# Optimization experiments

Hardware: AMD Instinct MI355X
Metric: run time of the kernel (lower is better)

## Reference

```python
import jax, jax.numpy as jnp
import numpy as np

EMBED = 1024
HEADS = 16
HDIM = EMBED // HEADS
MASK_OUT = -10000.0


def setup_inputs() -> dict:
    key = jax.random.key(0)
    ks = jax.random.split(key, 12)
    B, S = 4, 1023
    scale = 0.02
    return {
        "word_hidden_states": jax.random.normal(ks[0], (B, S, EMBED), jnp.float32),
        "image_hidden_states": jax.random.normal(ks[1], (B, EMBED), jnp.float32),
        "attention_mask": jnp.zeros((B, 1, 1, S), jnp.float32),
        "c_attn_w": jax.random.normal(ks[2], (EMBED, 3 * EMBED), jnp.float32) * scale,
        "c_attn_b": jnp.zeros((3 * EMBED,), jnp.float32),
        "c_proj_w": jax.random.normal(ks[3], (EMBED, EMBED), jnp.float32) * scale,
        "c_proj_b": jnp.zeros((EMBED,), jnp.float32),
        "uk_w": jax.random.normal(ks[4], (EMBED, EMBED), jnp.float32) * scale,
        "uk_b": jnp.zeros((EMBED,), jnp.float32),
        "uv_w": jax.random.normal(ks[5], (EMBED, EMBED), jnp.float32) * scale,
        "uv_b": jnp.zeros((EMBED,), jnp.float32),
    }


def _split_heads(t):
    # [B, T, E] -> [B, H, T, D]
    B, T, _ = t.shape
    return t.reshape(B, T, HEADS, HDIM).transpose(0, 2, 1, 3)


def reference(word_hidden_states, image_hidden_states, attention_mask,
              c_attn_w, c_attn_b, c_proj_w, c_proj_b,
              uk_w, uk_b, uv_w, uv_b):
    B, S, _ = word_hidden_states.shape
    # c_attn: Conv1D -> x @ W + b, then split into q, k, v
    qkv = word_hidden_states @ c_attn_w + c_attn_b          # [B, S, 3E]
    q_word, k_word, v_word = jnp.split(qkv, 3, axis=-1)
    # image key/value via nn.Linear (x @ W^T + b)
    img = image_hidden_states[:, None, :]                    # [B, 1, E]
    k_img = img @ uk_w.T + uk_b
    v_img = img @ uv_w.T + uv_b
    k = jnp.concatenate([k_img, k_word], axis=1)             # [B, S+1, E]
    v = jnp.concatenate([v_img, v_word], axis=1)

    q = _split_heads(q_word)                                 # [B, H, S, D]
    k = _split_heads(k)                                      # [B, H, S+1, D]
    v = _split_heads(v)

    scores = jnp.einsum("bhqd,bhkd->bhqk", q, k) / jnp.sqrt(jnp.float32(HDIM))
    # causal mask: tril rows [1 : S+1], cols [: S+1] of max_positions grid
    # -> query i may attend key j iff j <= i + 1 (image token always visible)
    qi = jnp.arange(S)[:, None]
    kj = jnp.arange(S + 1)[None, :]
    causal = kj <= qi + 1                                     # [S, S+1]
    scores = jnp.where(causal[None, None], scores, jnp.float32(MASK_OUT))
    # prepend zero column to additive attention mask for the image token
    zero_col = jnp.zeros(attention_mask.shape[:-1] + (1,), attention_mask.dtype)
    mask = jnp.concatenate([zero_col, attention_mask], axis=-1)  # [B,1,1,S+1]
    scores = scores + mask
    attn = jax.nn.softmax(scores, axis=-1)                    # dropout: eval mode (identity)
    out = jnp.einsum("bhqk,bhkd->bhqd", attn, v)              # [B, H, S, D]
    out = out.transpose(0, 2, 1, 3).reshape(B, S, EMBED)      # merge heads
    out = out @ c_proj_w + c_proj_b                           # c_proj Conv1D
    return out
```

## Files before the change

### kernel.cpp

```cpp
#include <hip/hip_runtime.h>

#define EMBED 1024
#define HEADS 16
#define HDIM 64
#define SQ 1023
#define SK 1024
#define MTOK 4092
#define MPAD 4096

typedef __attribute__((ext_vector_type(8))) short short8;
typedef __attribute__((ext_vector_type(4))) float floatx4;

static __device__ __forceinline__ unsigned short f2bf(float f) {
  union { float f; unsigned u; } v; v.f = f;
  unsigned u = v.u;
  u += 0x7fffu + ((u >> 16) & 1u);
  return (unsigned short)(u >> 16);
}
static __device__ __forceinline__ float bf2f(unsigned short s) {
  union { unsigned u; float f; } v; v.u = ((unsigned)s) << 16;
  return v.f;
}

static __device__ __forceinline__ void gld16(const unsigned short* g, unsigned short* l) {
  typedef const __attribute__((address_space(1))) unsigned int guint;
  typedef __attribute__((address_space(3))) unsigned int luint;
  __builtin_amdgcn_global_load_lds((guint*)(const void*)g, (luint*)(void*)l, 16, 0, 0);
}

__global__ __launch_bounds__(256) void k_prep(
    const float* __restrict__ word, const float* __restrict__ attn_w,
    const float* __restrict__ proj_w, const float* __restrict__ img,
    const float* __restrict__ ukw, const float* __restrict__ ukb,
    const float* __restrict__ uvw, const float* __restrict__ uvb,
    unsigned short* __restrict__ A, unsigned short* __restrict__ WtA,
    unsigned short* __restrict__ WtP, unsigned short* __restrict__ Qb,
    unsigned short* __restrict__ Kb, unsigned short* __restrict__ Vt) {
  __shared__ float T[32][33];
  int bx = blockIdx.x, t = threadIdx.x;
  if (bx < 2048) {
    int idx = (bx * 256 + t) * 8;
    int row = idx >> 10;
    short8 v;
    if (row < MTOK) {
      const float4* p = (const float4*)(word + idx);
      float4 a = p[0], b = p[1];
      v[0] = (short)f2bf(a.x); v[1] = (short)f2bf(a.y);
      v[2] = (short)f2bf(a.z); v[3] = (short)f2bf(a.w);
      v[4] = (short)f2bf(b.x); v[5] = (short)f2bf(b.y);
      v[6] = (short)f2bf(b.z); v[7] = (short)f2bf(b.w);
    } else {
#pragma unroll
      for (int i = 0; i < 8; i++) v[i] = 0;
    }
    *(short8*)(A + idx) = v;
  } else if (bx < 6144) {
    const float* W; unsigned short* Wt; int N, n0, k0;
    if (bx < 5120) {
      int r = bx - 2048; W = attn_w; Wt = WtA; N = 3072;
      n0 = (r % 96) * 32; k0 = (r / 96) * 32;
    } else {
      int r = bx - 5120; W = proj_w; Wt = WtP; N = 1024;
      n0 = (r & 31) * 32; k0 = (r >> 5) * 32;
    }
    int tx = t & 31, ty = t >> 5;
#pragma unroll
    for (int i = 0; i < 4; i++) {
      int r = ty + i * 8;
      T[r][tx] = W[(k0 + r) * N + n0 + tx];
    }
    __syncthreads();
#pragma unroll
    for (int i = 0; i < 4; i++) {
      int r = ty + i * 8;
      Wt[(n0 + r) * 1024 + k0 + tx] = f2bf(T[tx][r]);
    }
  } else if (bx < 8192) {
    int wid = (bx - 6144) * 4 + (t >> 6);
    int lane = t & 63;
    int which = wid >> 12;
    int bb = (wid >> 10) & 3;
    int n = wid & 1023;
    const float* W = which ? uvw : ukw;
    const float* bias = which ? uvb : ukb;
    const float* x = img + bb * 1024;
    const float* w = W + n * 1024;
    float s = 0.f;
#pragma unroll
    for (int i = 0; i < 16; i++) { int k = i * 64 + lane; s += x[k] * w[k]; }
#pragma unroll
    for (int off = 32; off; off >>= 1) s += __shfl_xor(s, off);
    if (lane == 0) {
      int h = n >> 6, d = n & 63;
      unsigned short val = f2bf(s + bias[n]);
      if (which == 0) Kb[((bb * HEADS + h) * SK + (SK - 1)) * HDIM + d] = val;
      else            Vt[((bb * HEADS + h) * HDIM + d) * SK + (SK - 1)] = val;
    }
  } else {
    int i = (bx - 8192) * 256 + t;
    int bh = i >> 6, d = i & 63;
    Qb[(bh * SK + (SK - 1)) * HDIM + d] = 0;
  }
}

template <int EPI, int TN>
__global__ __launch_bounds__(256, 2) void k_gemm(
    const unsigned short* __restrict__ A, const unsigned short* __restrict__ Bt,
    int Kdim, const float* __restrict__ bias,
    unsigned short* __restrict__ Qb, unsigned short* __restrict__ Kb,
    unsigned short* __restrict__ VtOut, float* __restrict__ out) {
  constexpr int NC = TN / 32;
  __shared__ __attribute__((aligned(16))) unsigned short Sm[8192 + TN * 64];
  unsigned short* As = Sm;
  unsigned short* Bs = Sm + 8192;
  int t = threadIdx.x, lane = t & 63, w = t >> 6;
  int quad = lane >> 4, l16 = lane & 15;
  int m0 = blockIdx.y * 128, n0 = blockIdx.x * TN;
  int waveM = (w >> 1) * 64, waveN = (w & 1) * (TN / 2);
  int rs = t >> 3, cs = t & 7;

  floatx4 acc[4][NC];
#pragma unroll
  for (int i = 0; i < 4; i++)
#pragma unroll
    for (int j = 0; j < NC; j++)
#pragma unroll
      for (int e = 0; e < 4; e++) acc[i][j][e] = 0.f;

  const unsigned short* Ag = A + m0 * Kdim;
  const unsigned short* Bg = Bt + n0 * Kdim;

  for (int k0 = 0; k0 < Kdim; k0 += 64) {
    __syncthreads();
#pragma unroll
    for (int i = 0; i < 4; i++) {
      int r = i * 32 + rs;
      gld16(Ag + r * Kdim + k0 + ((cs ^ (r & 7)) * 8), As + i * 2048 + t * 8);
    }
#pragma unroll
    for (int i = 0; i < TN / 32; i++) {
      int r = i * 32 + rs;
      gld16(Bg + r * Kdim + k0 + ((cs ^ (r & 7)) * 8), Bs + i * 2048 + t * 8);
    }
    __syncthreads();
#pragma unroll
    for (int kk = 0; kk < 2; kk++) {
      short8 af[4], bf8[NC];
#pragma unroll
      for (int mr = 0; mr < 4; mr++) {
        int row = waveM + mr * 16 + l16;
        af[mr] = *(const short8*)(As + row * 64 + (((kk * 4 + quad) ^ (row & 7)) * 8));
      }
#pragma unroll
      for (int nc = 0; nc < NC; nc++) {
        int row = waveN + nc * 16 + l16;
        bf8[nc] = *(const short8*)(Bs + row * 64 + (((kk * 4 + quad) ^ (row & 7)) * 8));
      }
#pragma unroll
      for (int mr = 0; mr < 4; mr++)
#pragma unroll
        for (int nc = 0; nc < NC; nc++)
          acc[mr][nc] = __builtin_amdgcn_mfma_f32_16x16x32_bf16(af[mr], bf8[nc], acc[mr][nc], 0, 0, 0);
    }
  }

  float bv[NC];
#pragma unroll
  for (int nc = 0; nc < NC; nc++) bv[nc] = bias[n0 + waveN + nc * 16 + l16];

  if (EPI == 0) {
    unsigned short* Cs = Sm;
    const int CST = 208;
    int startV = 2048 - n0;
    if (startV < 0) startV = 0;
    if (startV > TN) startV = TN;
    int chunksQK = startV >> 3;
    for (int p = 0; p < 2; p++) {
      __syncthreads();
      if ((w >> 1) == p) {
#pragma unroll
        for (int mr = 0; mr < 4; mr++)
#pragma unroll
          for (int nc = 0; nc < NC; nc++)
#pragma unroll
            for (int r = 0; r < 4; r++) {
              int lrow = mr * 16 + quad * 4 + r;
              int lcol = waveN + nc * 16 + l16;
              Cs[lrow * CST + (((lcol >> 3) ^ (quad << 1)) * 8) + (lcol & 7)] =
                  f2bf(acc[mr][nc][r] + bv[nc]);
            }
      }
      __syncthreads();
      {
        int lr = t & 63, gm = m0 + p * 64 + lr;
        int rot = ((lr >> 2) & 3) << 1;
        bool okm = (gm < MTOK);
        int bb = (unsigned)gm / 1023u;
        int s = gm - bb * 1023;
        for (int c8 = (t >> 6); c8 < chunksQK; c8 += 4) {
          short8 v = *(const short8*)(Cs + lr * CST + ((c8 ^ rot) * 8));
          int gn = n0 + c8 * 8;
          unsigned short* dst = (gn >> 10) ? Kb : Qb;
          int e = gn & 1023;
          int h = e >> 6, d0 = e & 63;
          if (okm) *(short8*)(dst + ((bb * HEADS + h) * SK + s) * HDIM + d0) = v;
        }
      }
      {
        int tok = t & 63, gm = m0 + p * 64 + tok;
        int rot = ((tok >> 2) & 3) << 1;
        bool okm = (gm < MTOK);
        int bb = (unsigned)gm / 1023u;
        int s = gm - bb * 1023;
        for (int c = startV + (t >> 6); c < TN; c += 4) {
          unsigned short val = Cs[tok * CST + (((c >> 3) ^ rot) * 8) + (c & 7)];
          int e = (n0 + c) & 1023;
          int h = e >> 6, d0 = e & 63;
          if (okm) VtOut[((bb * HEADS + h) * HDIM + d0) * SK + s] = val;
        }
      }
    }
  } else {
#pragma unroll
    for (int nc = 0; nc < NC; nc++) {
      int gn = n0 + waveN + nc * 16 + l16;
#pragma unroll
      for (int mr = 0; mr < 4; mr++) {
#pragma unroll
        for (int r = 0; r < 4; r++) {
          int gm = m0 + waveM + mr * 16 + quad * 4 + r;
          if (gm < MTOK) out[gm * EMBED + gn] = acc[mr][nc][r] + bv[nc];
        }
      }
    }
  }
}

__global__ __launch_bounds__(256, 2) void k_flash(
    const unsigned short* __restrict__ Qb, const unsigned short* __restrict__ Kb,
    const unsigned short* __restrict__ Vtg, const float* __restrict__ am,
    unsigned short* __restrict__ Ao) {
  __shared__ __attribute__((aligned(16))) unsigned short Ks[8192];
  __shared__ __attribute__((aligned(16))) unsigned short Vs[8192];
  __shared__ __attribute__((aligned(16))) unsigned short Ps[8192];

  int t = threadIdx.x, lane = t & 63, w = t >> 6;
  int quad = lane >> 4, l16 = lane & 15;
  int B = blockIdx.x;
  int bh = (B & 7) | (((B >> 3) & 7) << 3);
  int tq = 15 - (B >> 6);
  int bb = bh >> 4, h = bh & 15;

  const float SCL = 0.18033688011f;
  const float MASKV = -14426.950408f;
  const float L2E = 1.44269504089f;

  short8 qf[2];
  {
    int qrow = tq * 64 + w * 16 + l16;
#pragma unroll
    for (int kk = 0; kk < 2; kk++)
      qf[kk] = *(const short8*)(Qb + (bh * SK + qrow) * HDIM + (kk * 4 + quad) * 8);
  }

  float m_i[4], l_i[4];
  floatx4 acc_o[4];
  {
    float s0 = 0.f;
#pragma unroll
    for (int kk = 0; kk < 2; kk++) {
      short8 ki = *(const short8*)(Kb + (bh * SK + (SK - 1)) * HDIM + (kk * 4 + quad) * 8);
#pragma unroll
      for (int j = 0; j < 8; j++)
        s0 += bf2f((unsigned short)qf[kk][j]) * bf2f((unsigned short)ki[j]);
    }
    s0 += __shfl_xor(s0, 16);
    s0 += __shfl_xor(s0, 32);
    s0 *= SCL;
#pragma unroll
    for (int r = 0; r < 4; r++) {
      m_i[r] = __shfl(s0, quad * 4 + r);
      l_i[r] = 1.f;
    }
#pragma unroll
    for (int n = 0; n < 4; n++) {
      float vf = bf2f(Vtg[(bh * HDIM + n * 16 + l16) * SK + (SK - 1)]);
#pragma unroll
      for (int e = 0; e < 4; e++) acc_o[n][e] = vf;
    }
  }

  unsigned short* Pw = Ps + w * 2048;
  const float* amb = am + bb * SQ;
  int jmax = tq >> 1;

  for (int j = 0; j <= jmax; j++) {
    __syncthreads();
#pragma unroll
    for (int i = 0; i < 4; i++) {
      int r = i * 32 + (t >> 3), gc = (t & 7) ^ (r & 7);
      gld16(Kb + (bh * SK + j * 128 + r) * HDIM + gc * 8, Ks + i * 2048 + t * 8);
    }
#pragma unroll
    for (int i = 0; i < 4; i++) {
      int d = i * 16 + (t >> 4), gc = (t & 15) ^ (d & 7);
      gld16(Vtg + (bh * HDIM + d) * SK + j * 128 + gc * 8, Vs + i * 2048 + t * 8);
    }
    __syncthreads();

    bool diag = (j == jmax);
    int qmaxw = tq * 64 + w * 16 + 15;

    floatx4 sacc[8];
#pragma unroll
    for (int n = 0; n < 8; n++)
#pragma unroll
      for (int e = 0; e < 4; e++) sacc[n][e] = 0.f;
#pragma unroll
    for (int nc = 0; nc < 8; nc++) {
      if (j * 128 + nc * 16 <= qmaxw) {
        int krow = nc * 16 + l16;
#pragma unroll
        for (int kk = 0; kk < 2; kk++) {
          short8 b = *(const short8*)(Ks + krow * 64 + (((kk * 4 + quad) ^ (krow & 7)) * 8));
          sacc[nc] = __builtin_amdgcn_mfma_f32_16x16x32_bf16(qf[kk], b, sacc[nc], 0, 0, 0);
        }
      }
    }

    int qbase = tq * 64 + w * 16 + quad * 4;
    float tmax[4];
#pragma unroll
    for (int r = 0; r < 4; r++) tmax[r] = -1e30f;
#pragma unroll
    for (int nc = 0; nc < 8; nc++) {
      if (j * 128 + nc * 16 > qmaxw) {
#pragma unroll
        for (int r = 0; r < 4; r++) sacc[nc][r] = 0.f;
      } else {
        int s = j * 128 + nc * 16 + l16;
        float amv = (s < SQ) ? amb[s] * L2E : 0.f;
#pragma unroll
        for (int r = 0; r < 4; r++) {
          float sc = sacc[nc][r] * SCL;
          if (diag && s > qbase + r) sc = MASKV;
          sc += amv;
          sacc[nc][r] = sc;
          tmax[r] = fmaxf(tmax[r], sc);
        }
      }
    }
#pragma unroll
    for (int off = 1; off < 16; off <<= 1)
#pragma unroll
      for (int r = 0; r < 4; r++) tmax[r] = fmaxf(tmax[r], __shfl_xor(tmax[r], off));

    float alpha[4];
#pragma unroll
    for (int r = 0; r < 4; r++) {
      float mn = fmaxf(m_i[r], tmax[r]);
      alpha[r] = __builtin_amdgcn_exp2f(m_i[r] - mn);
      m_i[r] = mn;
    }
    float rsum[4] = {0.f, 0.f, 0.f, 0.f};
#pragma unroll
    for (int nc = 0; nc < 8; nc++) {
      if (j * 128 + nc * 16 <= qmaxw) {
#pragma unroll
        for (int r = 0; r < 4; r++) {
          float p = __builtin_amdgcn_exp2f(sacc[nc][r] - m_i[r]);
          sacc[nc][r] = p;
          rsum[r] += p;
        }
      }
    }
#pragma unroll
    for (int off = 1; off < 16; off <<= 1)
#pragma unroll
      for (int r = 0; r < 4; r++) rsum[r] += __shfl_xor(rsum[r], off);
#pragma unroll
    for (int r = 0; r < 4; r++) l_i[r] = l_i[r] * alpha[r] + rsum[r];
#pragma unroll
    for (int n = 0; n < 4; n++)
#pragma unroll
      for (int e = 0; e < 4; e++) acc_o[n][e] *= alpha[e];

#pragma unroll
    for (int nc = 0; nc < 8; nc++)
#pragma unroll
      for (int r = 0; r < 4; r++) {
        int row = quad * 4 + r;
        union { float f; unsigned u; } cv; cv.f = sacc[nc][r];
        Pw[row * 128 + (((nc * 2 + (l16 >> 3)) ^ (row & 7)) * 8) + (l16 & 7)] =
            (unsigned short)(cv.u >> 16);
      }

#pragma unroll
    for (int kk2 = 0; kk2 < 4; kk2++) {
      short8 a = *(const short8*)(Pw + l16 * 128 + (((kk2 * 4 + quad) ^ (l16 & 7)) * 8));
#pragma unroll
      for (int n = 0; n < 4; n++) {
        int vrow = n * 16 + l16;
        short8 b = *(const short8*)(Vs + vrow * 128 + (((kk2 * 4 + quad) ^ (vrow & 7)) * 8));
        acc_o[n] = __builtin_amdgcn_mfma_f32_16x16x32_bf16(a, b, acc_o[n], 0, 0, 0);
      }
    }
  }

  float inv[4];
#pragma unroll
  for (int r = 0; r < 4; r++) inv[r] = 1.f / l_i[r];
  unsigned short* Os = Ps;
  __syncthreads();
#pragma unroll
  for (int n = 0; n < 4; n++)
#pragma unroll
    for (int r = 0; r < 4; r++) {
      int row = w * 16 + quad * 4 + r, col = n * 16 + l16;
      Os[row * 64 + ((((col >> 3) + row) & 7) * 8) + (col & 7)] = f2bf(acc_o[n][r] * inv[r]);
    }
  __syncthreads();
#pragma unroll
  for (int i = 0; i < 2; i++) {
    int cid = i * 256 + t, r = cid >> 3, c8 = cid & 7;
    int q = tq * 64 + r;
    if (q < SQ) {
      short8 v = *(const short8*)(Os + r * 64 + (((c8 + r) & 7) * 8));
      *(short8*)(Ao + (bb * SQ + q) * EMBED + h * HDIM + c8 * 8) = v;
    }
  }
}

extern "C" void kernel_launch(void* const* d_in, const int* in_sizes, int n_in,
                              void* d_out, int out_size, void* d_ws, size_t ws_size,
                              hipStream_t stream) {
  const float* word   = (const float*)d_in[0];
  const float* img    = (const float*)d_in[1];
  const float* amask  = (const float*)d_in[2];
  const float* attn_w = (const float*)d_in[3];
  const float* attn_b = (const float*)d_in[4];
  const float* proj_w = (const float*)d_in[5];
  const float* proj_b = (const float*)d_in[6];
  const float* ukw    = (const float*)d_in[7];
  const float* ukb    = (const float*)d_in[8];
  const float* uvw    = (const float*)d_in[9];
  const float* uvb    = (const float*)d_in[10];
  float* out = (float*)d_out;

  char* ws = (char*)d_ws;
  unsigned short* Aw     = (unsigned short*)(ws);
  unsigned short* WtAttn = (unsigned short*)(ws + 8388608);
  unsigned short* WtProj = (unsigned short*)(ws + 14680064);
  unsigned short* Qb     = (unsigned short*)(ws + 16777216);
  unsigned short* Kb     = (unsigned short*)(ws + 25165824);
  unsigned short* Vtg    = (unsigned short*)(ws + 33554432);
  unsigned short* Ao     = Aw;

  k_prep<<<8208, 256, 0, stream>>>(word, attn_w, proj_w, img, ukw, ukb, uvw, uvb,
                                   Aw, WtAttn, WtProj, Qb, Kb, Vtg);
  k_gemm<0, 192><<<dim3(16, 32), 256, 0, stream>>>(Aw, WtAttn, 1024, attn_b, Qb, Kb, Vtg, nullptr);
  k_flash<<<1024, 256, 0, stream>>>(Qb, Kb, Vtg, amask, Ao);
  k_gemm<1, 128><<<dim3(8, 32), 256, 0, stream>>>(Ao, WtProj, 1024, proj_b, nullptr, nullptr, nullptr, out);
}
```

Baseline: 202.8 us.

## Double-buffer K/V tiles in flash attention and use DPP row reductions

```diff
diff --git a/kernel.cpp b/kernel.cpp
--- a/kernel.cpp
+++ b/kernel.cpp
@@ -26,6 +26,13 @@
   typedef const __attribute__((address_space(1))) unsigned int guint;
   typedef __attribute__((address_space(3))) unsigned int luint;
   __builtin_amdgcn_global_load_lds((guint*)(const void*)g, (luint*)(void*)l, 16, 0, 0);
+}
+
+template <int CTRL>
+static __device__ __forceinline__ float rorf(float x) {
+  union { float f; int i; } v; v.f = x;
+  v.i = __builtin_amdgcn_update_dpp(v.i, v.i, CTRL, 0xF, 0xF, true);
+  return v.f;
 }
 
 __global__ __launch_bounds__(256) void k_prep(
@@ -240,8 +247,8 @@
     const unsigned short* __restrict__ Qb, const unsigned short* __restrict__ Kb,
     const unsigned short* __restrict__ Vtg, const float* __restrict__ am,
     unsigned short* __restrict__ Ao) {
-  __shared__ __attribute__((aligned(16))) unsigned short Ks[8192];
-  __shared__ __attribute__((aligned(16))) unsigned short Vs[8192];
+  __shared__ __attribute__((aligned(16))) unsigned short Ks[16384];
+  __shared__ __attribute__((aligned(16))) unsigned short Vs[16384];
   __shared__ __attribute__((aligned(16))) unsigned short Ps[8192];
 
   int t = threadIdx.x, lane = t & 63, w = t >> 6;
@@ -294,19 +301,28 @@
   const float* amb = am + bb * SQ;
   int jmax = tq >> 1;
 
-  for (int j = 0; j <= jmax; j++) {
-    __syncthreads();
+  auto stage = [&](int j, int buf) {
+    unsigned short* Kd = Ks + buf * 8192;
+    unsigned short* Vd = Vs + buf * 8192;
 #pragma unroll
     for (int i = 0; i < 4; i++) {
       int r = i * 32 + (t >> 3), gc = (t & 7) ^ (r & 7);
-      gld16(Kb + (bh * SK + j * 128 + r) * HDIM + gc * 8, Ks + i * 2048 + t * 8);
+      gld16(Kb + (bh * SK + j * 128 + r) * HDIM + gc * 8, Kd + i * 2048 + t * 8);
     }
 #pragma unroll
     for (int i = 0; i < 4; i++) {
       int d = i * 16 + (t >> 4), gc = (t & 15) ^ (d & 7);
-      gld16(Vtg + (bh * HDIM + d) * SK + j * 128 + gc * 8, Vs + i * 2048 + t * 8);
-    }
+      gld16(Vtg + (bh * HDIM + d) * SK + j * 128 + gc * 8, Vd + i * 2048 + t * 8);
+    }
+  };
+
+  stage(0, 0);
+  for (int j = 0; j <= jmax; j++) {
+    int cur = j & 1;
     __syncthreads();
+    if (j < jmax) stage(j + 1, cur ^ 1);
+    const unsigned short* Kc = Ks + cur * 8192;
+    const unsigned short* Vc = Vs + cur * 8192;
 
     bool diag = (j == jmax);
     int qmaxw = tq * 64 + w * 16 + 15;
@@ -322,7 +338,7 @@
         int krow = nc * 16 + l16;
 #pragma unroll
         for (int kk = 0; kk < 2; kk++) {
-          short8 b = *(const short8*)(Ks + krow * 64 + (((kk * 4 + quad) ^ (krow & 7)) * 8));
+          short8 b = *(const short8*)(Kc + krow * 64 + (((kk * 4 + quad) ^ (krow & 7)) * 8));
           sacc[nc] = __builtin_amdgcn_mfma_f32_16x16x32_bf16(qf[kk], b, sacc[nc], 0, 0, 0);
         }
       }
@@ -351,9 +367,14 @@
       }
     }
 #pragma unroll
-    for (int off = 1; off < 16; off <<= 1)
-#pragma unroll
-      for (int r = 0; r < 4; r++) tmax[r] = fmaxf(tmax[r], __shfl_xor(tmax[r], off));
+    for (int r = 0; r < 4; r++) {
+      float o = tmax[r];
+      o = fmaxf(o, rorf<0x121>(o));
+      o = fmaxf(o, rorf<0x122>(o));
+      o = fmaxf(o, rorf<0x124>(o));
+      o = fmaxf(o, rorf<0x128>(o));
+      tmax[r] = o;
+    }
 
     float alpha[4];
 #pragma unroll
@@ -375,9 +396,14 @@
       }
     }
 #pragma unroll
-    for (int off = 1; off < 16; off <<= 1)
-#pragma unroll
-      for (int r = 0; r < 4; r++) rsum[r] += __shfl_xor(rsum[r], off);
+    for (int r = 0; r < 4; r++) {
+      float o = rsum[r];
+      o += rorf<0x121>(o);
+      o += rorf<0x122>(o);
+      o += rorf<0x124>(o);
+      o += rorf<0x128>(o);
+      rsum[r] = o;
+    }
 #pragma unroll
     for (int r = 0; r < 4; r++) l_i[r] = l_i[r] * alpha[r] + rsum[r];
 #pragma unroll
@@ -401,7 +427,7 @@
 #pragma unroll
       for (int n = 0; n < 4; n++) {
         int vrow = n * 16 + l16;
-        short8 b = *(const short8*)(Vs + vrow * 128 + (((kk2 * 4 + quad) ^ (vrow & 7)) * 8));
+        short8 b = *(const short8*)(Vc + vrow * 128 + (((kk2 * 4 + quad) ^ (vrow & 7)) * 8));
         acc_o[n] = __builtin_amdgcn_mfma_f32_16x16x32_bf16(a, b, acc_o[n], 0, 0, 0);
       }
     }
```

Result: slower. 312.7 us (+54.2%).
